# Kernel optimization log

Hardware: AMD Instinct MI355X
Metric: run time of the kernel (lower is better)

## Reference

```python
import jax, jax.numpy as jnp
import numpy as np

INTERVAL = 8
HEADS = 4
DIM = 64


def grid_shuffle(x, I):
    # rearrange 'b c (h i) (w j) -> (b i j) c h w' : stride-I residue grouping
    B, C, H, W = x.shape
    h, w = H // I, W // I
    x = x.reshape(B, C, h, I, w, I).transpose(0, 3, 5, 1, 2, 4)
    return x.reshape(B * I * I, C, h, w)


def grid_unshuffle(x, I, B):
    Bp, C, h, w = x.shape
    x = x.reshape(B, I, I, C, h, w).transpose(0, 3, 4, 1, 5, 2)
    return x.reshape(B, C, h * I, w * I)


def conv1x1(x, w, b):
    return jnp.einsum('oc,bchw->bohw', w, x) + b[None, :, None, None]


def pos_bias(h, w, W1, b1, W2, b2):
    # dynamic RPE: MLP over normalized relative coordinates -> [heads, N, N]
    ch = jnp.arange(h)
    cw = jnp.arange(w)
    coords = jnp.stack(jnp.meshgrid(ch, cw, indexing='ij'), -1).reshape(-1, 2).astype(jnp.float32)
    denom = jnp.array([max(h - 1, 1), max(w - 1, 1)], dtype=jnp.float32)
    rel = (coords[:, None, :] - coords[None, :, :]) / denom  # [N,N,2]
    hid = jax.nn.relu(rel @ W1 + b1)
    bias = hid @ W2 + b2  # [N,N,heads]
    return bias.transpose(2, 0, 1)


def mask_attn(q2d, k2d, v2d, bias, pw, pb, heads, scale):
    Bp, C, h, w = q2d.shape
    N, d = h * w, C // heads

    def to_tok(t):  # [Bp,C,h,w] -> [Bp,heads,N,d]
        return t.reshape(Bp, heads, d, N).transpose(0, 1, 3, 2)

    q, k, v = to_tok(q2d), to_tok(k2d), to_tok(v2d)
    attn = jnp.einsum('bhnd,bhmd->bhnm', q * scale, k) + bias[None]
    attn = jax.nn.softmax(attn, axis=-1)
    out = jnp.einsum('bhnm,bhmd->bhnd', attn, v)
    out2d = out.transpose(0, 1, 3, 2).reshape(Bp, C, h, w)
    return conv1x1(out2d, pw, pb)


def setup_inputs() -> dict:
    key = jax.random.key(0)
    ks = jax.random.split(key, 14)
    pos_hidden = DIM // 4  # 16
    s = 0.02
    return {
        'x': jax.random.normal(ks[0], (2, DIM, 160, 160), jnp.float32),
        'qkv_w': jax.random.normal(ks[1], (3 * DIM, DIM), jnp.float32) * s,
        'qkv_b': jnp.zeros((3 * DIM,), jnp.float32),
        'grid_w': jax.random.normal(ks[2], (DIM, DIM), jnp.float32) * s,
        'grid_b': jnp.zeros((DIM,), jnp.float32),
        'pos_w1': jax.random.normal(ks[3], (2, pos_hidden), jnp.float32) * s,
        'pos_b1': jnp.zeros((pos_hidden,), jnp.float32),
        'pos_w2': jax.random.normal(ks[4], (pos_hidden, HEADS), jnp.float32) * s,
        'pos_b2': jnp.zeros((HEADS,), jnp.float32),
        'proj1_w': jax.random.normal(ks[5], (DIM, DIM), jnp.float32) * s,
        'proj1_b': jnp.zeros((DIM,), jnp.float32),
        'proj2_w': jax.random.normal(ks[6], (DIM, DIM), jnp.float32) * s,
        'proj2_b': jnp.zeros((DIM,), jnp.float32),
    }


def reference(x, qkv_w, qkv_b, grid_w, grid_b, pos_w1, pos_b1, pos_w2, pos_b2,
              proj1_w, proj1_b, proj2_w, proj2_b):
    I = INTERVAL
    scale = (DIM // HEADS) ** -0.5
    B, C, H, W = x.shape
    qkv = conv1x1(x, qkv_w, qkv_b)
    x_grid = conv1x1(grid_shuffle(x, I), grid_w, grid_b)
    qkv = grid_shuffle(qkv, I)
    bias = pos_bias(H // I, W // I, pos_w1, pos_b1, pos_w2, pos_b2)
    q, k, v = jnp.split(qkv, 3, axis=1)
    out = mask_attn(x_grid, k, v, bias, proj1_w, proj1_b, HEADS, scale)
    out = mask_attn(q, x_grid, out, bias, proj2_w, proj2_b, HEADS, scale)
    return grid_unshuffle(out, I, B)
```

## Files before the change

### kernel.cpp

```cpp
#include <hip/hip_runtime.h>
#include <hip/hip_bf16.h>


#define N_TOK 400
#define NP    416
#define BP    128

typedef short bf16x8 __attribute__((ext_vector_type(8)));
typedef float f32x16 __attribute__((ext_vector_type(16)));

__device__ inline ushort f2bf(float f) {
    __hip_bfloat16 h = __float2bfloat16(f);
    return *reinterpret_cast<ushort*>(&h);
}
__device__ inline float bf2f(ushort u) {
    union { uint i; float f; } v; v.i = (uint)u << 16; return v.f;
}
__device__ inline uint pk2(float a, float b) {
    return (uint)f2bf(a) | ((uint)f2bf(b) << 16);
}
__device__ inline bf16x8 ld16(const ushort* p) {
    union { uint4 q; bf16x8 v; } u;
    u.q = *reinterpret_cast<const uint4*>(p);
    return u.v;
}
__device__ inline float fast_exp2(float x) {
#if __has_builtin(__builtin_amdgcn_exp2f)
    return __builtin_amdgcn_exp2f(x);
#else
    return __expf(x * 0.6931471805599453f);
#endif
}
__device__ inline float fast_rcp(float x) {
#if __has_builtin(__builtin_amdgcn_rcpf)
    return __builtin_amdgcn_rcpf(x);
#else
    return 1.0f / x;
#endif
}

#define L2E 1.4426950408889634f
#define QK_PRESCALE 0.36067376022224085f

__global__ __launch_bounds__(256) void k_prep(
    const float* __restrict__ W1, const float* __restrict__ B1,
    const float* __restrict__ W2, const float* __restrict__ B2,
    const float* __restrict__ qkv_w, const float* __restrict__ qkv_b,
    const float* __restrict__ grid_w, const float* __restrict__ grid_b,
    const float* __restrict__ p1w, const float* __restrict__ p2w,
    float* __restrict__ biasF, ushort* __restrict__ Wc, float* __restrict__ Bc,
    ushort* __restrict__ Wp1, ushort* __restrict__ Wp2)
{
    int blk = blockIdx.x;
    if (blk < 2704) {
        int idx = blk * 256 + threadIdx.x;
        if (idx >= 692224) return;
        int r = idx & 15, lane = (idx >> 4) & 63;
        int tile = idx >> 10;
        int mt = tile % 13, rem = tile / 13, qt = rem % 13, h = rem / 13;
        int n = qt * 32 + (lane & 31);
        int m = mt * 32 + (r & 3) + 8 * (r >> 2) + 4 * (lane >> 5);
        float val = 0.0f;
        if (n < 400 && m < 400) {
            float r0 = (float)(n / 20 - m / 20) * (1.0f / 19.0f);
            float r1 = (float)(n % 20 - m % 20) * (1.0f / 19.0f);
            float o = B2[h];
#pragma unroll
            for (int k = 0; k < 16; ++k) {
                float hh = r0 * W1[k] + r1 * W1[16 + k] + B1[k];
                hh = fmaxf(hh, 0.0f);
                o += hh * W2[k * 4 + h];
            }
            val = o * L2E;
        }
        biasF[idx] = val;
    } else {
        int t = (blk - 2704) * 256 + threadIdx.x;
        if (t < 16384) {
            int oc = t >> 6, k = t & 63;
            float v = (oc < 192) ? qkv_w[oc * 64 + k] : grid_w[(oc - 192) * 64 + k];
            Wc[t] = f2bf(v);
        } else if (t < 16384 + 4096) {
            Wp1[t - 16384] = f2bf(p1w[t - 16384]);
        } else if (t < 16384 + 8192) {
            Wp2[t - 16384 - 4096] = f2bf(p2w[t - 16384 - 4096]);
        } else if (t < 16384 + 8192 + 256) {
            int oc = t - 16384 - 8192;
            Bc[oc] = (oc < 192) ? qkv_b[oc] : grid_b[oc - 192];
        }
    }
}

__global__ __launch_bounds__(256) void k_conv(
    const float* __restrict__ x, const ushort* __restrict__ Wc,
    const float* __restrict__ Bc,
    ushort* __restrict__ Qb, ushort* __restrict__ Kb,
    ushort* __restrict__ Vb, ushort* __restrict__ XGb)
{
    __shared__ __align__(16) ushort XL[32 * 64];
    int blk = blockIdx.x;
    int b = blk / 800, rem = blk % 800;
    int H0 = rem / 5, wt = rem % 5;
    int w0 = wt * 32;
    int tid = threadIdx.x;

    {
        int c = tid >> 2, q4 = tid & 3;
        const float* xr = x + ((size_t)(b * 64 + c) * 160 + H0) * 160 + w0 + q4 * 8;
        float4 f0 = *reinterpret_cast<const float4*>(xr);
        float4 f1 = *reinterpret_cast<const float4*>(xr + 4);
        char* base = reinterpret_cast<char*>(XL);
#pragma unroll
        for (int k = 0; k < 8; ++k) {
            float v = (k < 4) ? ((const float*)&f0)[k] : ((const float*)&f1)[k - 4];
            int p = q4 * 8 + k;
            int byt = p * 128 + ((2 * c) ^ ((p & 7) << 4));
            *reinterpret_cast<ushort*>(base + byt) = f2bf(v);
        }
    }

    int lane = tid & 63, w = tid >> 6;
    int l31 = lane & 31, hi = lane >> 5;

    bf16x8 wf[2][4];
#pragma unroll
    for (int nt = 0; nt < 2; ++nt)
#pragma unroll
        for (int kk = 0; kk < 4; ++kk)
            wf[nt][kk] = ld16(&Wc[(size_t)(w * 64 + nt * 32 + l31) * 64 + kk * 16 + hi * 8]);
    __syncthreads();

    f32x16 acc0 = 0.0f, acc1 = 0.0f;
    const char* base = reinterpret_cast<const char*>(XL);
#pragma unroll
    for (int kk = 0; kk < 4; ++kk) {
        int byt = l31 * 128 + (((kk * 32 + hi * 16)) ^ ((l31 & 7) << 4));
        bf16x8 xf;
        {
            union { uint4 q; bf16x8 v; } u;
            u.q = *reinterpret_cast<const uint4*>(base + byt);
            xf = u.v;
        }
        acc0 = __builtin_amdgcn_mfma_f32_32x32x16_bf16(wf[0][kk], xf, acc0, 0, 0, 0);
        acc1 = __builtin_amdgcn_mfma_f32_32x32x16_bf16(wf[1][kk], xf, acc1, 0, 0, 0);
    }

    int W0 = w0 + l31, ww = W0 >> 3, j = W0 & 7;
    int bp = b * 64 + (H0 & 7) * 8 + j;
    int n  = (H0 >> 3) * 20 + ww;
    ushort* outb = (w == 0) ? Qb : (w == 1) ? Kb : (w == 2) ? Vb : XGb;
    float mul = (w <= 1) ? QK_PRESCALE : 1.0f;
    ushort* dst = outb + ((size_t)bp * NP + n) * 64;
#pragma unroll
    for (int nt = 0; nt < 2; ++nt) {
        const f32x16& a = nt ? acc1 : acc0;
#pragma unroll
        for (int g = 0; g < 4; ++g) {
            int cc = nt * 32 + 8 * g + 4 * hi;
            int oc = w * 64 + cc;
            uint2 uu;
            uu.x = pk2((a[4 * g + 0] + Bc[oc + 0]) * mul, (a[4 * g + 1] + Bc[oc + 1]) * mul);
            uu.y = pk2((a[4 * g + 2] + Bc[oc + 2]) * mul, (a[4 * g + 3] + Bc[oc + 3]) * mul);
            *reinterpret_cast<uint2*>(dst + cc) = uu;
        }
    }
}

__global__ __launch_bounds__(512, 4) void k_attn_mfma(
    const ushort* __restrict__ Qg, const ushort* __restrict__ Kg,
    const ushort* __restrict__ Vg, const float* __restrict__ biasF,
    ushort* __restrict__ O)
{
    __shared__ ushort Ks[NP * 16];
    __shared__ ushort Vt[16 * 424];
    int blk = blockIdx.x;
    int bp = blk >> 3, h = (blk >> 1) & 3, sub = blk & 1;
    int qt0 = sub ? 7 : 0;
    int cnt = sub ? 6 : 7;
    int tid = threadIdx.x;

    const ushort* Ksrc = Kg + (size_t)bp * NP * 64 + h * 16;
#pragma unroll
    for (int it = 0; it < 2; ++it) {
        int i = tid + it * 512;
        if (i < NP * 2) {
            int row = i >> 1, half = i & 1;
            *reinterpret_cast<uint4*>(&Ks[row * 16 + half * 8]) =
                *reinterpret_cast<const uint4*>(&Ksrc[(size_t)row * 64 + half * 8]);
        }
    }
    const ushort* Vsrc = Vg + (size_t)bp * NP * 64 + h * 16;
#pragma unroll
    for (int it = 0; it < 2; ++it) {
        int i = tid + it * 512;
        if (i < 800) {
            int row = i >> 1, hf = i & 1;
            uint4 v = *reinterpret_cast<const uint4*>(&Vsrc[(size_t)row * 64 + hf * 8]);
            const ushort* pv = reinterpret_cast<const ushort*>(&v);
#pragma unroll
            for (int k = 0; k < 8; ++k)
                Vt[(hf * 8 + k) * 424 + row] = pv[k];
        }
    }
    __syncthreads();

    int lane = tid & 63, w = tid >> 6;
    int l31 = lane & 31, hi = lane >> 5;

    if (w >= cnt) return;
    int qt = qt0 + w;
    int qbase = qt * 32;
    bf16x8 qf = ld16(&Qg[((size_t)bp * NP + qbase + l31) * 64 + h * 16 + hi * 8]);
    f32x16 acc = 0.0f;
    const f32x16* bfr = reinterpret_cast<const f32x16*>(
        biasF + ((size_t)(h * 169 + qt * 13)) * 1024 + lane * 16);

    f32x16 cb = bfr[0];

#pragma unroll
    for (int mt = 0; mt < 13; ++mt) {
        const int mbase = mt * 32;
        f32x16 nb;
        if (mt < 12) nb = bfr[mt + 1];

        bf16x8 kf = ld16(&Ks[(mbase + l31) * 16 + hi * 8]);
        f32x16 sv = __builtin_amdgcn_mfma_f32_32x32x16_bf16(kf, qf, cb, 0, 0, 0);

        const int nv = (mt == 12) ? 8 : 16;
        float p[16];
#pragma unroll
        for (int r = 0; r < 16; ++r)
            if (r < nv) p[r] = fast_exp2(sv[r]);

        {
            uint c4 = pk2(p[0], p[1]), c5 = pk2(p[2], p[3]);
            uint c6 = pk2(p[4], p[5]), c7 = pk2(p[6], p[7]);
            asm("v_permlane32_swap_b32 %0, %1" : "+v"(c4), "+v"(c6));
            asm("v_permlane32_swap_b32 %0, %1" : "+v"(c5), "+v"(c7));
            union { uint u[4]; bf16x8 v; } A;
            A.u[0] = c4; A.u[1] = c5; A.u[2] = c6; A.u[3] = c7;
            bf16x8 vf;
            if (l31 < 16) vf = ld16(&Vt[l31 * 424 + mbase + hi * 8]);
            else { union { uint u[4]; bf16x8 v; } o; o.u[0]=o.u[1]=o.u[2]=o.u[3]=0x3F803F80u; vf = o.v; }
            acc = __builtin_amdgcn_mfma_f32_32x32x16_bf16(A.v, vf, acc, 0, 0, 0);
        }
        if (mt < 12) {
            uint c4 = pk2(p[8], p[9]),  c5 = pk2(p[10], p[11]);
            uint c6 = pk2(p[12], p[13]), c7 = pk2(p[14], p[15]);
            asm("v_permlane32_swap_b32 %0, %1" : "+v"(c4), "+v"(c6));
            asm("v_permlane32_swap_b32 %0, %1" : "+v"(c5), "+v"(c7));
            union { uint u[4]; bf16x8 v; } A;
            A.u[0] = c4; A.u[1] = c5; A.u[2] = c6; A.u[3] = c7;
            bf16x8 vf;
            if (l31 < 16) vf = ld16(&Vt[l31 * 424 + mbase + 16 + hi * 8]);
            else { union { uint u[4]; bf16x8 v; } o; o.u[0]=o.u[1]=o.u[2]=o.u[3]=0x3F803F80u; vf = o.v; }
            acc = __builtin_amdgcn_mfma_f32_32x32x16_bf16(A.v, vf, acc, 0, 0, 0);
        }
        cb = nb;
    }

#pragma unroll
    for (int r = 0; r < 16; ++r) {
        int moff = (r & 3) + 8 * (r >> 2) + 4 * hi;
        int q = qbase + moff;
        float s = __shfl(acc[r], lane | 16);
        if (l31 < 16 && q < N_TOK)
            O[((size_t)bp * 400 + q) * 64 + h * 16 + l31] = f2bf(acc[r] * fast_rcp(s));
    }
}

template<int MODE>
__global__ __launch_bounds__(256) void k_proj(
    const ushort* __restrict__ In, const ushort* __restrict__ Wp,
    const float* __restrict__ Bv, ushort* __restrict__ Out)
{
    __shared__ __align__(16) ushort XL[128 * 64];
    size_t t0 = (size_t)blockIdx.x * 128;
    int tid = threadIdx.x;

    char* basec = reinterpret_cast<char*>(XL);
#pragma unroll
    for (int it = 0; it < 4; ++it) {
        int idx = tid + it * 256;
        int p = idx >> 3, c8 = idx & 7;
        uint4 v = *reinterpret_cast<const uint4*>(In + (t0 + p) * 64 + c8 * 8);
        int byt = p * 128 + ((c8 * 16) ^ ((p & 7) << 4));
        *reinterpret_cast<uint4*>(basec + byt) = v;
    }

    int lane = tid & 63, w = tid >> 6;
    int l31 = lane & 31, hi = lane >> 5;

    bf16x8 wf[2][4];
#pragma unroll
    for (int nt = 0; nt < 2; ++nt)
#pragma unroll
        for (int kk = 0; kk < 4; ++kk)
            wf[nt][kk] = ld16(&Wp[(size_t)(nt * 32 + l31) * 64 + kk * 16 + hi * 8]);
    __syncthreads();

    int prow = w * 32 + l31;
    f32x16 acc0 = 0.0f, acc1 = 0.0f;
#pragma unroll
    for (int kk = 0; kk < 4; ++kk) {
        int byt = prow * 128 + (((kk * 32 + hi * 16)) ^ ((prow & 7) << 4));
        union { uint4 q; bf16x8 v; } u;
        u.q = *reinterpret_cast<const uint4*>(basec + byt);
        acc0 = __builtin_amdgcn_mfma_f32_32x32x16_bf16(wf[0][kk], u.v, acc0, 0, 0, 0);
        acc1 = __builtin_amdgcn_mfma_f32_32x32x16_bf16(wf[1][kk], u.v, acc1, 0, 0, 0);
    }

    size_t t = t0 + prow;
    ushort* dst;
    if (MODE == 0) {
        int bp = (int)(t / 400), n = (int)(t % 400);
        dst = Out + ((size_t)bp * NP + n) * 64;
    } else {
        dst = Out + t * 64;
    }
#pragma unroll
    for (int nt = 0; nt < 2; ++nt) {
        const f32x16& a = nt ? acc1 : acc0;
#pragma unroll
        for (int g = 0; g < 4; ++g) {
            int cc = nt * 32 + 8 * g + 4 * hi;
            uint2 uu;
            uu.x = pk2(a[4 * g + 0] + Bv[cc + 0], a[4 * g + 1] + Bv[cc + 1]);
            uu.y = pk2(a[4 * g + 2] + Bv[cc + 2], a[4 * g + 3] + Bv[cc + 3]);
            *reinterpret_cast<uint2*>(dst + cc) = uu;
        }
    }
}

__global__ __launch_bounds__(256) void k_unshuffle(
    const ushort* __restrict__ In, float* __restrict__ out)
{
    __shared__ __align__(16) ushort il[160 * 64];
    int blk = blockIdx.x;
    int b = blk / 160, rem = blk % 160, iI = rem / 20, hh = rem % 20;
    int tid = threadIdx.x;

    for (int idx = tid; idx < 1280; idx += 256) {
        int j = idx / 160, r2 = idx % 160, ww = r2 / 8, c8 = r2 % 8;
        int bp = b * 64 + iI * 8 + j;
        int n  = hh * 20 + ww;
        uint4 v = reinterpret_cast<const uint4*>(In + ((size_t)bp * 400 + n) * 64)[c8];
        reinterpret_cast<uint4*>(&il[(ww * 8 + j) * 64])[c8] = v;
    }
    __syncthreads();

    int c = tid >> 2, q = tid & 3;
    int H0 = hh * 8 + iI;
    float* og = out + ((size_t)(b * 64 + c) * 160 + H0) * 160;
#pragma unroll
    for (int k = 0; k < 10; ++k) {
        int f = q + 4 * k;
        float4 v;
        v.x = bf2f(il[(4 * f + 0) * 64 + c]);
        v.y = bf2f(il[(4 * f + 1) * 64 + c]);
        v.z = bf2f(il[(4 * f + 2) * 64 + c]);
        v.w = bf2f(il[(4 * f + 3) * 64 + c]);
        reinterpret_cast<float4*>(og)[f] = v;
    }
}

extern "C" void kernel_launch(void* const* d_in, const int* in_sizes, int n_in,
                              void* d_out, int out_size, void* d_ws, size_t ws_size,
                              hipStream_t stream)
{
    const float* x      = (const float*)d_in[0];
    const float* qkv_w  = (const float*)d_in[1];
    const float* qkv_b  = (const float*)d_in[2];
    const float* grid_w = (const float*)d_in[3];
    const float* grid_b = (const float*)d_in[4];
    const float* pw1    = (const float*)d_in[5];
    const float* pb1    = (const float*)d_in[6];
    const float* pw2    = (const float*)d_in[7];
    const float* pb2    = (const float*)d_in[8];
    const float* p1w    = (const float*)d_in[9];
    const float* p1b    = (const float*)d_in[10];
    const float* p2w    = (const float*)d_in[11];
    const float* p2b    = (const float*)d_in[12];

    char* W = (char*)d_ws;
    float*  biasF = (float*)(W + 0);
    ushort* Wc    = (ushort*)(W + 2768896);
    ushort* Wp1   = (ushort*)(W + 2801664);
    ushort* Wp2   = (ushort*)(W + 2809856);
    float*  Bc    = (float*) (W + 2818048);
    const size_t BASE2 = 2819072;
    const size_t BB = (size_t)BP * NP * 64 * 2;
    ushort* Qb = (ushort*)(W + BASE2);
    ushort* Kb = (ushort*)(W + BASE2 + 1 * BB);
    ushort* Vb = (ushort*)(W + BASE2 + 2 * BB);
    ushort* XG = (ushort*)(W + BASE2 + 3 * BB);
    ushort* P1 = (ushort*)(W + BASE2 + 4 * BB);
    const size_t OB = (size_t)BP * 400 * 64 * 2;
    ushort* O1 = (ushort*)(W + BASE2 + 5 * BB);
    ushort* O2 = (ushort*)(W + BASE2 + 5 * BB + OB);
    ushort* OFb = O1;
    float*  out = (float*)d_out;

    k_prep<<<2801, 256, 0, stream>>>(pw1, pb1, pw2, pb2, qkv_w, qkv_b, grid_w, grid_b,
                                     p1w, p2w, biasF, Wc, Bc, Wp1, Wp2);
    k_conv<<<1600, 256, 0, stream>>>(x, Wc, Bc, Qb, Kb, Vb, XG);
    k_attn_mfma<<<1024, 512, 0, stream>>>(XG, Kb, Vb, biasF, O1);
    k_proj<0><<<400, 256, 0, stream>>>(O1, Wp1, p1b, P1);
    k_attn_mfma<<<1024, 512, 0, stream>>>(Qb, XG, P1, biasF, O2);
    k_proj<1><<<400, 256, 0, stream>>>(O2, Wp2, p2b, OFb);
    k_unshuffle<<<320, 256, 0, stream>>>(OFb, out);
}
```

Before: 127.2 us.

## Process multiple query tiles per wave to reuse K/V fragments in attention

The attention kernel now launches one 256-thread block per (batch, head) instead of two 512-thread blocks. Each of the 4 waves handles 3-4 query tiles at once, so each K and V fragment read from LDS is reused across several independent MFMA chains. This cuts the K/V staging in LDS to once per (batch, head) and amortizes shared-memory reads. The costs are more registers from four live accumulators, fewer blocks and waves in flight, and load imbalance because wave 0 carries an extra tile.

New measurement: 132.2 us. 4.0% more time.

```diff
diff --git a/kernel.cpp b/kernel.cpp
--- a/kernel.cpp
+++ b/kernel.cpp
@@ -166,7 +166,7 @@
     }
 }
 
-__global__ __launch_bounds__(512, 4) void k_attn_mfma(
+__global__ __launch_bounds__(256) void k_attn_mfma(
     const ushort* __restrict__ Qg, const ushort* __restrict__ Kg,
     const ushort* __restrict__ Vg, const float* __restrict__ biasF,
     ushort* __restrict__ O)
@@ -174,99 +174,141 @@
     __shared__ ushort Ks[NP * 16];
     __shared__ ushort Vt[16 * 424];
     int blk = blockIdx.x;
-    int bp = blk >> 3, h = (blk >> 1) & 3, sub = blk & 1;
-    int qt0 = sub ? 7 : 0;
-    int cnt = sub ? 6 : 7;
+    int bp = blk >> 2, h = blk & 3;
     int tid = threadIdx.x;
 
     const ushort* Ksrc = Kg + (size_t)bp * NP * 64 + h * 16;
-#pragma unroll
-    for (int it = 0; it < 2; ++it) {
-        int i = tid + it * 512;
-        if (i < NP * 2) {
-            int row = i >> 1, half = i & 1;
-            *reinterpret_cast<uint4*>(&Ks[row * 16 + half * 8]) =
-                *reinterpret_cast<const uint4*>(&Ksrc[(size_t)row * 64 + half * 8]);
-        }
+    for (int i = tid; i < NP * 2; i += 256) {
+        int row = i >> 1, half = i & 1;
+        *reinterpret_cast<uint4*>(&Ks[row * 16 + half * 8]) =
+            *reinterpret_cast<const uint4*>(&Ksrc[(size_t)row * 64 + half * 8]);
     }
     const ushort* Vsrc = Vg + (size_t)bp * NP * 64 + h * 16;
-#pragma unroll
-    for (int it = 0; it < 2; ++it) {
-        int i = tid + it * 512;
-        if (i < 800) {
-            int row = i >> 1, hf = i & 1;
-            uint4 v = *reinterpret_cast<const uint4*>(&Vsrc[(size_t)row * 64 + hf * 8]);
-            const ushort* pv = reinterpret_cast<const ushort*>(&v);
-#pragma unroll
-            for (int k = 0; k < 8; ++k)
-                Vt[(hf * 8 + k) * 424 + row] = pv[k];
-        }
+    for (int i = tid; i < 800; i += 256) {
+        int row = i >> 1, hf = i & 1;
+        uint4 v = *reinterpret_cast<const uint4*>(&Vsrc[(size_t)row * 64 + hf * 8]);
+        const ushort* pv = reinterpret_cast<const ushort*>(&v);
+#pragma unroll
+        for (int k = 0; k < 8; ++k)
+            Vt[(hf * 8 + k) * 424 + row] = pv[k];
     }
     __syncthreads();
 
     int lane = tid & 63, w = tid >> 6;
     int l31 = lane & 31, hi = lane >> 5;
 
-    if (w >= cnt) return;
-    int qt = qt0 + w;
-    int qbase = qt * 32;
-    bf16x8 qf = ld16(&Qg[((size_t)bp * NP + qbase + l31) * 64 + h * 16 + hi * 8]);
-    f32x16 acc = 0.0f;
-    const f32x16* bfr = reinterpret_cast<const f32x16*>(
-        biasF + ((size_t)(h * 169 + qt * 13)) * 1024 + lane * 16);
-
-    f32x16 cb = bfr[0];
-
-#pragma unroll
-    for (int mt = 0; mt < 13; ++mt) {
+    const int qt0 = w, qt1 = w + 4, qt2 = w + 8;
+    const int qt3 = (w == 0) ? 12 : w;
+    const bool has3 = (w == 0);
+
+    const size_t qrow = (size_t)bp * NP;
+    bf16x8 qf0 = ld16(&Qg[(qrow + qt0 * 32 + l31) * 64 + h * 16 + hi * 8]);
+    bf16x8 qf1 = ld16(&Qg[(qrow + qt1 * 32 + l31) * 64 + h * 16 + hi * 8]);
+    bf16x8 qf2 = ld16(&Qg[(qrow + qt2 * 32 + l31) * 64 + h * 16 + hi * 8]);
+    bf16x8 qf3 = ld16(&Qg[(qrow + qt3 * 32 + l31) * 64 + h * 16 + hi * 8]);
+
+    const float* bbase = biasF + (size_t)h * 169 * 1024 + lane * 16;
+    const f32x16* bf0 = reinterpret_cast<const f32x16*>(bbase + (size_t)qt0 * 13 * 1024);
+    const f32x16* bf1 = reinterpret_cast<const f32x16*>(bbase + (size_t)qt1 * 13 * 1024);
+    const f32x16* bf2 = reinterpret_cast<const f32x16*>(bbase + (size_t)qt2 * 13 * 1024);
+    const f32x16* bf3 = reinterpret_cast<const f32x16*>(bbase + (size_t)qt3 * 13 * 1024);
+
+    f32x16 a0 = 0.0f, a1 = 0.0f, a2 = 0.0f, a3 = 0.0f;
+
+    const uint ONE2 = 0x3F803F80u;
+
+#define QK_CHAIN(ACC, BFR, QF)                                                     \
+    do {                                                                           \
+        f32x16 cb_ = (BFR)[mt];                                                    \
+        f32x16 sv_ = __builtin_amdgcn_mfma_f32_32x32x16_bf16(kf, QF, cb_, 0, 0, 0);\
+        float p_[16];                                                              \
+        _Pragma("unroll") for (int r_ = 0; r_ < 16; ++r_) p_[r_] = fast_exp2(sv_[r_]); \
+        {                                                                          \
+            uint c0 = pk2(p_[0], p_[1]), c1 = pk2(p_[2], p_[3]);                   \
+            uint c2 = pk2(p_[4], p_[5]), c3 = pk2(p_[6], p_[7]);                   \
+            asm("v_permlane32_swap_b32 %0, %1" : "+v"(c0), "+v"(c2));              \
+            asm("v_permlane32_swap_b32 %0, %1" : "+v"(c1), "+v"(c3));              \
+            union { uint u[4]; bf16x8 v; } A_;                                     \
+            A_.u[0] = c0; A_.u[1] = c1; A_.u[2] = c2; A_.u[3] = c3;                \
+            ACC = __builtin_amdgcn_mfma_f32_32x32x16_bf16(A_.v, vf0, ACC, 0, 0, 0);\
+        }                                                                          \
+        {                                                                          \
+            uint c0 = pk2(p_[8], p_[9]),  c1 = pk2(p_[10], p_[11]);                \
+            uint c2 = pk2(p_[12], p_[13]), c3 = pk2(p_[14], p_[15]);               \
+            asm("v_permlane32_swap_b32 %0, %1" : "+v"(c0), "+v"(c2));              \
+            asm("v_permlane32_swap_b32 %0, %1" : "+v"(c1), "+v"(c3));              \
+            union { uint u[4]; bf16x8 v; } A_;                                     \
+            A_.u[0] = c0; A_.u[1] = c1; A_.u[2] = c2; A_.u[3] = c3;                \
+            ACC = __builtin_amdgcn_mfma_f32_32x32x16_bf16(A_.v, vf1, ACC, 0, 0, 0);\
+        }                                                                          \
+    } while (0)
+
+    for (int mt = 0; mt < 12; ++mt) {
         const int mbase = mt * 32;
-        f32x16 nb;
-        if (mt < 12) nb = bfr[mt + 1];
-
         bf16x8 kf = ld16(&Ks[(mbase + l31) * 16 + hi * 8]);
-        f32x16 sv = __builtin_amdgcn_mfma_f32_32x32x16_bf16(kf, qf, cb, 0, 0, 0);
-
-        const int nv = (mt == 12) ? 8 : 16;
-        float p[16];
-#pragma unroll
-        for (int r = 0; r < 16; ++r)
-            if (r < nv) p[r] = fast_exp2(sv[r]);
-
-        {
-            uint c4 = pk2(p[0], p[1]), c5 = pk2(p[2], p[3]);
-            uint c6 = pk2(p[4], p[5]), c7 = pk2(p[6], p[7]);
-            asm("v_permlane32_swap_b32 %0, %1" : "+v"(c4), "+v"(c6));
-            asm("v_permlane32_swap_b32 %0, %1" : "+v"(c5), "+v"(c7));
-            union { uint u[4]; bf16x8 v; } A;
-            A.u[0] = c4; A.u[1] = c5; A.u[2] = c6; A.u[3] = c7;
-            bf16x8 vf;
-            if (l31 < 16) vf = ld16(&Vt[l31 * 424 + mbase + hi * 8]);
-            else { union { uint u[4]; bf16x8 v; } o; o.u[0]=o.u[1]=o.u[2]=o.u[3]=0x3F803F80u; vf = o.v; }
-            acc = __builtin_amdgcn_mfma_f32_32x32x16_bf16(A.v, vf, acc, 0, 0, 0);
-        }
-        if (mt < 12) {
-            uint c4 = pk2(p[8], p[9]),  c5 = pk2(p[10], p[11]);
-            uint c6 = pk2(p[12], p[13]), c7 = pk2(p[14], p[15]);
-            asm("v_permlane32_swap_b32 %0, %1" : "+v"(c4), "+v"(c6));
-            asm("v_permlane32_swap_b32 %0, %1" : "+v"(c5), "+v"(c7));
-            union { uint u[4]; bf16x8 v; } A;
-            A.u[0] = c4; A.u[1] = c5; A.u[2] = c6; A.u[3] = c7;
-            bf16x8 vf;
-            if (l31 < 16) vf = ld16(&Vt[l31 * 424 + mbase + 16 + hi * 8]);
-            else { union { uint u[4]; bf16x8 v; } o; o.u[0]=o.u[1]=o.u[2]=o.u[3]=0x3F803F80u; vf = o.v; }
-            acc = __builtin_amdgcn_mfma_f32_32x32x16_bf16(A.v, vf, acc, 0, 0, 0);
-        }
-        cb = nb;
-    }
-
-#pragma unroll
-    for (int r = 0; r < 16; ++r) {
-        int moff = (r & 3) + 8 * (r >> 2) + 4 * hi;
-        int q = qbase + moff;
-        float s = __shfl(acc[r], lane | 16);
-        if (l31 < 16 && q < N_TOK)
-            O[((size_t)bp * 400 + q) * 64 + h * 16 + l31] = f2bf(acc[r] * fast_rcp(s));
-    }
+        bf16x8 vf0, vf1;
+        if (l31 < 16) {
+            vf0 = ld16(&Vt[l31 * 424 + mbase + hi * 8]);
+            vf1 = ld16(&Vt[l31 * 424 + mbase + 16 + hi * 8]);
+        } else {
+            union { uint u[4]; bf16x8 v; } o;
+            o.u[0] = o.u[1] = o.u[2] = o.u[3] = ONE2;
+            vf0 = o.v; vf1 = o.v;
+        }
+        QK_CHAIN(a0, bf0, qf0);
+        QK_CHAIN(a1, bf1, qf1);
+        QK_CHAIN(a2, bf2, qf2);
+        if (has3) QK_CHAIN(a3, bf3, qf3);
+    }
+
+    {
+        bf16x8 kf = ld16(&Ks[(384 + l31) * 16 + hi * 8]);
+        bf16x8 vf0;
+        if (l31 < 16) vf0 = ld16(&Vt[l31 * 424 + 384 + hi * 8]);
+        else { union { uint u[4]; bf16x8 v; } o; o.u[0]=o.u[1]=o.u[2]=o.u[3]=ONE2; vf0 = o.v; }
+
+#define QK_TAIL(ACC, BFR, QF)                                                      \
+        do {                                                                       \
+            f32x16 cb_ = (BFR)[12];                                                \
+            f32x16 sv_ = __builtin_amdgcn_mfma_f32_32x32x16_bf16(kf, QF, cb_, 0, 0, 0); \
+            float p_[8];                                                           \
+            _Pragma("unroll") for (int r_ = 0; r_ < 8; ++r_) p_[r_] = fast_exp2(sv_[r_]); \
+            uint c0 = pk2(p_[0], p_[1]), c1 = pk2(p_[2], p_[3]);                   \
+            uint c2 = pk2(p_[4], p_[5]), c3 = pk2(p_[6], p_[7]);                   \
+            asm("v_permlane32_swap_b32 %0, %1" : "+v"(c0), "+v"(c2));              \
+            asm("v_permlane32_swap_b32 %0, %1" : "+v"(c1), "+v"(c3));              \
+            union { uint u[4]; bf16x8 v; } A_;                                     \
+            A_.u[0] = c0; A_.u[1] = c1; A_.u[2] = c2; A_.u[3] = c3;                \
+            ACC = __builtin_amdgcn_mfma_f32_32x32x16_bf16(A_.v, vf0, ACC, 0, 0, 0);\
+        } while (0)
+
+        QK_TAIL(a0, bf0, qf0);
+        QK_TAIL(a1, bf1, qf1);
+        QK_TAIL(a2, bf2, qf2);
+        if (has3) QK_TAIL(a3, bf3, qf3);
+    }
+
+#define STORE_CHAIN(ACC, QT)                                                       \
+    do {                                                                           \
+        int qbase_ = (QT) * 32;                                                    \
+        _Pragma("unroll") for (int r_ = 0; r_ < 16; ++r_) {                        \
+            int moff_ = (r_ & 3) + 8 * (r_ >> 2) + 4 * hi;                         \
+            int q_ = qbase_ + moff_;                                               \
+            float s_ = __shfl(ACC[r_], lane | 16);                                 \
+            if (l31 < 16 && q_ < N_TOK)                                            \
+                O[((size_t)bp * 400 + q_) * 64 + h * 16 + l31] =                   \
+                    f2bf(ACC[r_] * fast_rcp(s_));                                  \
+        }                                                                          \
+    } while (0)
+
+    STORE_CHAIN(a0, qt0);
+    STORE_CHAIN(a1, qt1);
+    STORE_CHAIN(a2, qt2);
+    if (has3) STORE_CHAIN(a3, qt3);
+
+#undef QK_CHAIN
+#undef QK_TAIL
+#undef STORE_CHAIN
 }
 
 template<int MODE>
@@ -404,9 +446,9 @@
     k_prep<<<2801, 256, 0, stream>>>(pw1, pb1, pw2, pb2, qkv_w, qkv_b, grid_w, grid_b,
                                      p1w, p2w, biasF, Wc, Bc, Wp1, Wp2);
     k_conv<<<1600, 256, 0, stream>>>(x, Wc, Bc, Qb, Kb, Vb, XG);
-    k_attn_mfma<<<1024, 512, 0, stream>>>(XG, Kb, Vb, biasF, O1);
+    k_attn_mfma<<<512, 256, 0, stream>>>(XG, Kb, Vb, biasF, O1);
     k_proj<0><<<400, 256, 0, stream>>>(O1, Wp1, p1b, P1);
-    k_attn_mfma<<<1024, 512, 0, stream>>>(Qb, XG, P1, biasF, O2);
+    k_attn_mfma<<<512, 256, 0, stream>>>(Qb, XG, P1, biasF, O2);
     k_proj<1><<<400, 256, 0, stream>>>(O2, Wp2, p2b, OFb);
     k_unshuffle<<<320, 256, 0, stream>>>(OFb, out);
 }
```
